# Performance work log

Measured on AMD Instinct MI355X. Metric: run time of the kernel, lower is better.

## Reference

```python
import jax, jax.numpy as jnp
import numpy as np

D_IN = 1024
D_OUT = 1024
NUM_HEADS = 16
HEAD_DIM = D_OUT // NUM_HEADS


def setup_inputs() -> dict:
    key = jax.random.key(0)
    ks = jax.random.split(key, 6)
    b, T = 2, 2048
    scale = 0.02
    x = jax.random.normal(ks[0], (b, T, D_IN), dtype=jnp.float32)
    Wq = jax.random.normal(ks[1], (D_IN, D_OUT), dtype=jnp.float32) * scale
    Wk = jax.random.normal(ks[2], (D_IN, D_OUT), dtype=jnp.float32) * scale
    Wv = jax.random.normal(ks[3], (D_IN, D_OUT), dtype=jnp.float32) * scale
    Wo = jax.random.normal(ks[4], (D_OUT, D_OUT), dtype=jnp.float32) * scale
    bo = jnp.zeros((D_OUT,), dtype=jnp.float32)
    return {"x": x, "Wq": Wq, "Wk": Wk, "Wv": Wv, "Wo": Wo, "bo": bo}


def reference(x, Wq, Wk, Wv, Wo, bo):
    b, T, _ = x.shape
    H, Dh = NUM_HEADS, HEAD_DIM
    # projections: [b,T,d_out] -> [b,H,T,Dh]
    q = (x @ Wq).reshape(b, T, H, Dh).transpose(0, 2, 1, 3)
    k = (x @ Wk).reshape(b, T, H, Dh).transpose(0, 2, 1, 3)
    v = (x @ Wv).reshape(b, T, H, Dh).transpose(0, 2, 1, 3)
    # scores: [b,H,T,T]
    att = jnp.einsum('bhqd,bhkd->bhqk', q, k)
    causal = jnp.triu(jnp.ones((T, T), dtype=bool), k=1)
    att = jnp.where(causal, -jnp.inf, att)
    att = jax.nn.softmax(att / np.sqrt(Dh).astype(np.float32), axis=-1)
    # dropout p=0.0 -> identity
    y = jnp.einsum('bhqk,bhkd->bhqd', att, v)
    y = y.transpose(0, 2, 1, 3).reshape(b, T, H * Dh)
    return y @ Wo + bo
```

## Files before the change

kernel.cpp:

```cpp
#include <hip/hip_runtime.h>

#define T_   2048
#define DM   1024
#define H_   16
#define DH   64

typedef unsigned short u16;
typedef unsigned int u32;
typedef __attribute__((ext_vector_type(8))) short bf16x8;
typedef __attribute__((ext_vector_type(8))) unsigned short u16x8;
typedef __attribute__((ext_vector_type(4))) float f32x4;
typedef __attribute__((ext_vector_type(16))) float f32x16;
typedef __attribute__((ext_vector_type(4))) unsigned int u32x4;
typedef __attribute__((ext_vector_type(2))) unsigned int u32x2;

static __device__ __forceinline__ u16 f2b(float f) {
  unsigned int u = __builtin_bit_cast(unsigned int, f);
  u += 0x7fff + ((u >> 16) & 1);
  return (u16)(u >> 16);
}

static __device__ __forceinline__ u32 cvtpk(float a, float b) {
  u32 d;
  asm("v_cvt_pk_bf16_f32 %0, %1, %2" : "=v"(d) : "v"(a), "v"(b));
  return d;
}

static __device__ __forceinline__ void gll16(const void* g, void* l) {
  __builtin_amdgcn_global_load_lds(
      (const __attribute__((address_space(1))) unsigned int*)g,
      (__attribute__((address_space(3))) unsigned int*)l, 16, 0, 0);
}

static __device__ __forceinline__ bf16x8 ldf(const char* base, int rho,
                                             int k16) {
  return *(const bf16x8*)(base + rho * 128 + ((k16 ^ (rho & 7)) << 4));
}


__global__ __launch_bounds__(256) void k_cvt_x(const float* __restrict__ x,
                                               u16* __restrict__ o) {
  int i = (blockIdx.x * 256 + threadIdx.x) * 8;
  float4 a = *(const float4*)(x + i);
  float4 b = *(const float4*)(x + i + 4);
  u16x8 r;
  r[0] = f2b(a.x); r[1] = f2b(a.y); r[2] = f2b(a.z); r[3] = f2b(a.w);
  r[4] = f2b(b.x); r[5] = f2b(b.y); r[6] = f2b(b.z); r[7] = f2b(b.w);
  *(u16x8*)(o + i) = r;
}

__global__ __launch_bounds__(256) void k_cvt_wt(
    const float* __restrict__ Wq, const float* __restrict__ Wk,
    const float* __restrict__ Wv, const float* __restrict__ Wo,
    u16* __restrict__ oq, u16* __restrict__ ok, u16* __restrict__ ov,
    u16* __restrict__ oo) {
  const float* W; u16* Wt;
  int z = blockIdx.z;
  if (z == 0)      { W = Wq; Wt = oq; }
  else if (z == 1) { W = Wk; Wt = ok; }
  else if (z == 2) { W = Wv; Wt = ov; }
  else             { W = Wo; Wt = oo; }
  const float wsc = (z == 0) ? 0.1803368801111204f : 1.0f;
  __shared__ u16 tile[64][65];
  int k0 = blockIdx.x * 64, n0 = blockIdx.y * 64;
  int r = threadIdx.x >> 2, c0 = (threadIdx.x & 3) * 16;
  const float* src = W + (k0 + r) * DM + n0 + c0;
#pragma unroll
  for (int e = 0; e < 16; e += 4) {
    float4 v = *(const float4*)(src + e);
    tile[r][c0 + e + 0] = f2b(v.x * wsc);
    tile[r][c0 + e + 1] = f2b(v.y * wsc);
    tile[r][c0 + e + 2] = f2b(v.z * wsc);
    tile[r][c0 + e + 3] = f2b(v.w * wsc);
  }
  __syncthreads();
  u16x8 a, b;
#pragma unroll
  for (int e = 0; e < 8; ++e) a[e] = tile[c0 + e][r];
#pragma unroll
  for (int e = 0; e < 8; ++e) b[e] = tile[c0 + 8 + e][r];
  u16* dst = Wt + (n0 + r) * DM + k0 + c0;
  *(u16x8*)dst = a;
  *(u16x8*)(dst + 8) = b;
}

__global__ __launch_bounds__(256) void k_qkv(
    const u16* __restrict__ X, const u16* __restrict__ Wqt,
    const u16* __restrict__ Wkt, const u16* __restrict__ Wvt,
    u16* __restrict__ Qg, u16* __restrict__ Kg, u16* __restrict__ Vtg) {
  __shared__ char smem[34816];
  char* As = smem;
  char* Bs = smem + 16384;
  const int tid = threadIdx.x, lane = tid & 63, w = tid >> 6;
  const int frow = lane & 15, fk = lane >> 4;
  const int wr = (w >> 1) * 64, wc = (w & 1) * 64;
  const int m0 = blockIdx.x * 128;
  const int by = blockIdx.y;
  const int z = by >> 3, n0 = (by & 7) * 128;
  const u16* Wt = (z == 0) ? Wqt : (z == 1) ? Wkt : Wvt;
  const u16* Ap = X + m0 * DM;
  const u16* Bp = Wt + n0 * DM;
  const int ro = lane >> 3;
  const int ce = ((lane & 7) ^ ro) << 3;

  f32x4 acc[4][4];
#pragma unroll
  for (int mi = 0; mi < 4; ++mi)
#pragma unroll
    for (int ni = 0; ni < 4; ++ni) acc[mi][ni] = (f32x4){0.f, 0.f, 0.f, 0.f};

  for (int k0 = 0; k0 < DM; k0 += 64) {
#pragma unroll
    for (int c = 0; c < 4; ++c) {
      const int g8 = (w * 4 + c) * 8;
      gll16(Ap + (g8 + ro) * DM + k0 + ce, As + g8 * 128);
      gll16(Bp + (g8 + ro) * DM + k0 + ce, Bs + g8 * 128);
    }
    asm volatile("s_waitcnt vmcnt(0)" ::: "memory");
    __syncthreads();
    bf16x8 a[4][2], b[4][2];
#pragma unroll
    for (int mi = 0; mi < 4; ++mi)
#pragma unroll
      for (int kk = 0; kk < 2; ++kk)
        a[mi][kk] = ldf(As, wr + mi * 16 + frow, kk * 4 + fk);
#pragma unroll
    for (int ni = 0; ni < 4; ++ni)
#pragma unroll
      for (int kk = 0; kk < 2; ++kk)
        b[ni][kk] = ldf(Bs, wc + ni * 16 + frow, kk * 4 + fk);
#pragma unroll
    for (int mi = 0; mi < 4; ++mi)
#pragma unroll
      for (int ni = 0; ni < 4; ++ni)
#pragma unroll
        for (int kk = 0; kk < 2; ++kk)
          acc[mi][ni] = __builtin_amdgcn_mfma_f32_16x16x32_bf16(
              a[mi][kk], b[ni][kk], acc[mi][ni], 0, 0, 0);
    __syncthreads();
  }

  if (z < 2) {
    u16* out = (z == 0) ? Qg : Kg;
#pragma unroll
    for (int mi = 0; mi < 4; ++mi)
#pragma unroll
      for (int ni = 0; ni < 4; ++ni)
#pragma unroll
        for (int r = 0; r < 4; ++r) {
          int m = m0 + wr + mi * 16 + fk * 4 + r;
          int nl = n0 + wc + ni * 16 + frow;
          int b = m >> 11, t = m & 2047, h = nl >> 6, d = nl & 63;
          out[((b * H_ + h) * T_ + t) * DH + d] = f2b(acc[mi][ni][r]);
        }
  } else {
    u16* Tl = (u16*)smem;
#pragma unroll
    for (int ni = 0; ni < 4; ++ni) {
      const int n = wc + ni * 16 + frow;
#pragma unroll
      for (int mi = 0; mi < 4; ++mi)
#pragma unroll
        for (int r = 0; r < 4; ++r)
          Tl[n * 136 + wr + mi * 16 + fk * 4 + r] = f2b(acc[mi][ni][r]);
    }
    __syncthreads();
    const int n = tid >> 1, c0 = (tid & 1) * 64;
    const int ng = n0 + n, h = ng >> 6, d = ng & 63;
    const int b = m0 >> 11;
    const int tb = (m0 & 2047) + c0;
    u16* dst = Vtg + ((b * H_ + h) * DH + d) * T_ + tb;
#pragma unroll
    for (int e = 0; e < 8; ++e)
      *(u16x8*)(dst + e * 8) = *(const u16x8*)(Tl + n * 136 + c0 + e * 8);
  }
}

__global__ __launch_bounds__(256) void k_out(
    const u16* __restrict__ Y, const u16* __restrict__ Wot,
    const float* __restrict__ bo, float* __restrict__ out) {
  __shared__ char smem[24576];
  char* As = smem;
  char* Bs = smem + 8192;
  const int tid = threadIdx.x, lane = tid & 63, w = tid >> 6;
  const int frow = lane & 15, fk = lane >> 4;
  const int wr = (w >> 1) * 32, wc = (w & 1) * 64;
  const int m0 = blockIdx.x * 64, n0 = blockIdx.y * 128;
  const u16* Ap = Y + m0 * DM;
  const u16* Bp = Wot + n0 * DM;
  const int ro = lane >> 3;
  const int ce = ((lane & 7) ^ ro) << 3;

  f32x4 acc[2][4];
#pragma unroll
  for (int mi = 0; mi < 2; ++mi)
#pragma unroll
    for (int ni = 0; ni < 4; ++ni) acc[mi][ni] = (f32x4){0.f, 0.f, 0.f, 0.f};

  for (int k0 = 0; k0 < DM; k0 += 64) {
#pragma unroll
    for (int c = 0; c < 2; ++c) {
      const int g8 = (w * 2 + c) * 8;
      gll16(Ap + (g8 + ro) * DM + k0 + ce, As + g8 * 128);
    }
#pragma unroll
    for (int c = 0; c < 4; ++c) {
      const int g8 = (w * 4 + c) * 8;
      gll16(Bp + (g8 + ro) * DM + k0 + ce, Bs + g8 * 128);
    }
    asm volatile("s_waitcnt vmcnt(0)" ::: "memory");
    __syncthreads();
    bf16x8 a[2][2], b[4][2];
#pragma unroll
    for (int mi = 0; mi < 2; ++mi)
#pragma unroll
      for (int kk = 0; kk < 2; ++kk)
        a[mi][kk] = ldf(As, wr + mi * 16 + frow, kk * 4 + fk);
#pragma unroll
    for (int ni = 0; ni < 4; ++ni)
#pragma unroll
      for (int kk = 0; kk < 2; ++kk)
        b[ni][kk] = ldf(Bs, wc + ni * 16 + frow, kk * 4 + fk);
#pragma unroll
    for (int mi = 0; mi < 2; ++mi)
#pragma unroll
      for (int ni = 0; ni < 4; ++ni)
#pragma unroll
        for (int kk = 0; kk < 2; ++kk)
          acc[mi][ni] = __builtin_amdgcn_mfma_f32_16x16x32_bf16(
              a[mi][kk], b[ni][kk], acc[mi][ni], 0, 0, 0);
    __syncthreads();
  }
#pragma unroll
  for (int mi = 0; mi < 2; ++mi)
#pragma unroll
    for (int ni = 0; ni < 4; ++ni)
#pragma unroll
      for (int r = 0; r < 4; ++r) {
        int m = m0 + wr + mi * 16 + fk * 4 + r;
        int n = n0 + wc + ni * 16 + frow;
        out[m * DM + n] = acc[mi][ni][r] + bo[n];
      }
}

__global__ __launch_bounds__(256) void k_attn(
    const u16* __restrict__ Qg, const u16* __restrict__ Kg,
    const u16* __restrict__ Vtg, u16* __restrict__ Yg) {
  __shared__ char Kl[64 * 128];
  __shared__ char Vl[64 * 128];
  const int bh = blockIdx.x;
  const int qt = 15 - blockIdx.y;
  const int q0 = qt * 128;
  const int tid = threadIdx.x, w = tid >> 6, lane = tid & 63;
  const int hi = lane >> 5, qq = lane & 31;
  const u16* Qb = Qg + bh * (T_ * DH);
  const u16* Kb = Kg + bh * (T_ * DH);
  const u16* Vb = Vtg + bh * (DH * T_);
  const int qrow = q0 + w * 32 + qq;

  bf16x8 qf[4];
#pragma unroll
  for (int kb = 0; kb < 4; ++kb)
    qf[kb] = *(const bf16x8*)(Qb + qrow * DH + kb * 16 + hi * 8);

  f32x16 o0, o1;
#pragma unroll
  for (int r = 0; r < 16; ++r) { o0[r] = 0.f; o1[r] = 0.f; }
  float m = -1e30f, lp = 0.f;

  const int nt = 2 * qt + 2;
  const int nfull = 2 * qt + (w >> 1);
  const int sr = tid >> 3, sc = tid & 7;
  const int swz0 = (sr * 128 + sc * 16) ^ ((sr & 7) << 4);
  const int swz1 = ((sr + 32) * 128 + sc * 16) ^ ((sr & 7) << 4);

  u32x4 kr0 = *(const u32x4*)(Kb + sr * DH + sc * 8);
  u32x4 kr1 = *(const u32x4*)(Kb + (sr + 32) * DH + sc * 8);
  u32x4 vr0 = *(const u32x4*)(Vb + sr * T_ + sc * 8);
  u32x4 vr1 = *(const u32x4*)(Vb + (sr + 32) * T_ + sc * 8);

  for (int t = 0; t < nt; ++t) {
    __syncthreads();
    *(u32x4*)(Kl + swz0) = kr0;
    *(u32x4*)(Kl + swz1) = kr1;
    *(u32x4*)(Vl + swz0) = vr0;
    *(u32x4*)(Vl + swz1) = vr1;
    __syncthreads();
    if (t + 1 < nt) {
      const int jn = (t + 1) * 64;
      kr0 = *(const u32x4*)(Kb + (jn + sr) * DH + sc * 8);
      kr1 = *(const u32x4*)(Kb + (jn + sr + 32) * DH + sc * 8);
      vr0 = *(const u32x4*)(Vb + sr * T_ + jn + sc * 8);
      vr1 = *(const u32x4*)(Vb + (sr + 32) * T_ + jn + sc * 8);
    }
    if (t > nfull) continue;
    const int j0 = t * 64;

    f32x16 s0, s1;
#pragma unroll
    for (int r = 0; r < 16; ++r) { s0[r] = 0.f; s1[r] = 0.f; }
#pragma unroll
    for (int kb = 0; kb < 4; ++kb) {
      const int cb = (kb * 2 + hi) * 16;
      bf16x8 ka0 = *(const bf16x8*)(Kl + ((qq * 128 + cb) ^ ((qq & 7) << 4)));
      s0 = __builtin_amdgcn_mfma_f32_32x32x16_bf16(ka0, qf[kb], s0, 0, 0, 0);
      bf16x8 ka1 =
          *(const bf16x8*)(Kl + (((qq + 32) * 128 + cb) ^ ((qq & 7) << 4)));
      s1 = __builtin_amdgcn_mfma_f32_32x32x16_bf16(ka1, qf[kb], s1, 0, 0, 0);
    }
    if (t == nfull) {
#pragma unroll
      for (int r = 0; r < 16; ++r) {
        const int cr = (r & 3) + 8 * (r >> 2) + 4 * hi;
        if (j0 + cr > qrow) s0[r] = -1e30f;
        if (j0 + 32 + cr > qrow) s1[r] = -1e30f;
      }
    }
    float mt = s0[0];
#pragma unroll
    for (int r = 1; r < 16; ++r) mt = fmaxf(mt, s0[r]);
#pragma unroll
    for (int r = 0; r < 16; ++r) mt = fmaxf(mt, s1[r]);
    mt = fmaxf(mt, __shfl_xor(mt, 32));
    if (__any(mt > m + 8.f)) {
      const float mn = fmaxf(m, mt);
      const float al = __builtin_amdgcn_exp2f(m - mn);
      m = mn;
#pragma unroll
      for (int r = 0; r < 16; ++r) { o0[r] *= al; o1[r] *= al; }
      lp *= al;
    }
#pragma unroll
    for (int r = 0; r < 16; ++r) {
      s0[r] = __builtin_amdgcn_exp2f(s0[r] - m);
      s1[r] = __builtin_amdgcn_exp2f(s1[r] - m);
    }
    float ps = 0.f;
#pragma unroll
    for (int r = 0; r < 16; ++r) ps += s0[r] + s1[r];
    lp += ps;
    bf16x8 pb[4];
#define MKCH(DST, S, RB)                                                     \
  {                                                                          \
    u32 a01 = cvtpk(S[RB + 0], S[RB + 1]);                                   \
    u32 a23 = cvtpk(S[RB + 2], S[RB + 3]);                                   \
    u32 a45 = cvtpk(S[RB + 4], S[RB + 5]);                                   \
    u32 a67 = cvtpk(S[RB + 6], S[RB + 7]);                                   \
    asm volatile("v_permlane32_swap_b32 %0, %1" : "+v"(a01), "+v"(a45));     \
    asm volatile("v_permlane32_swap_b32 %0, %1" : "+v"(a23), "+v"(a67));     \
    u32x4 t4;                                                                \
    t4[0] = a01; t4[1] = a23; t4[2] = a45; t4[3] = a67;                      \
    DST = __builtin_bit_cast(bf16x8, t4);                                    \
  }
    MKCH(pb[0], s0, 0)
    MKCH(pb[1], s0, 8)
    MKCH(pb[2], s1, 0)
    MKCH(pb[3], s1, 8)
#undef MKCH
#pragma unroll
    for (int jc = 0; jc < 4; ++jc) {
      const int cb = (jc * 2 + hi) * 16;
      bf16x8 va0 = *(const bf16x8*)(Vl + ((qq * 128 + cb) ^ ((qq & 7) << 4)));
      o0 = __builtin_amdgcn_mfma_f32_32x32x16_bf16(va0, pb[jc], o0, 0, 0, 0);
      bf16x8 va1 =
          *(const bf16x8*)(Vl + (((qq + 32) * 128 + cb) ^ ((qq & 7) << 4)));
      o1 = __builtin_amdgcn_mfma_f32_32x32x16_bf16(va1, pb[jc], o1, 0, 0, 0);
    }
  }
  lp += __shfl_xor(lp, 32);
  const float rl = 1.0f / lp;
  const int obase = ((bh >> 4) * T_ + qrow) * DM + (bh & 15) * DH;
#pragma unroll
  for (int g = 0; g < 4; ++g) {
    u32x2 st;
    st[0] = cvtpk(o0[g * 4 + 0] * rl, o0[g * 4 + 1] * rl);
    st[1] = cvtpk(o0[g * 4 + 2] * rl, o0[g * 4 + 3] * rl);
    *(u32x2*)(Yg + obase + g * 8 + hi * 4) = st;
    st[0] = cvtpk(o1[g * 4 + 0] * rl, o1[g * 4 + 1] * rl);
    st[1] = cvtpk(o1[g * 4 + 2] * rl, o1[g * 4 + 3] * rl);
    *(u32x2*)(Yg + obase + 32 + g * 8 + hi * 4) = st;
  }
}


extern "C" void kernel_launch(void* const* d_in, const int* in_sizes, int n_in,
                              void* d_out, int out_size, void* d_ws,
                              size_t ws_size, hipStream_t stream) {
  const float* x  = (const float*)d_in[0];
  const float* Wq = (const float*)d_in[1];
  const float* Wk = (const float*)d_in[2];
  const float* Wv = (const float*)d_in[3];
  const float* Wo = (const float*)d_in[4];
  const float* bo = (const float*)d_in[5];
  float* out = (float*)d_out;
  char* ws = (char*)d_ws;

  u16* xb  = (u16*)(ws);
  u16* wqt = (u16*)(ws + (8ull << 20));
  u16* wkt = (u16*)(ws + (10ull << 20));
  u16* wvt = (u16*)(ws + (12ull << 20));
  u16* wot = (u16*)(ws + (14ull << 20));
  u16* Qg  = (u16*)(ws + (16ull << 20));
  u16* Kg  = (u16*)(ws + (24ull << 20));
  u16* Vtg = (u16*)(ws + (32ull << 20));
  u16* Yg  = (u16*)(ws + (40ull << 20));

  k_cvt_x<<<2048, 256, 0, stream>>>(x, xb);
  k_cvt_wt<<<dim3(16, 16, 4), 256, 0, stream>>>(Wq, Wk, Wv, Wo, wqt, wkt, wvt, wot);
  k_qkv<<<dim3(32, 24), 256, 0, stream>>>(xb, wqt, wkt, wvt, Qg, Kg, Vtg);
  k_attn<<<dim3(32, 16), 256, 0, stream>>>(Qg, Kg, Vtg, Yg);
  k_out<<<dim3(64, 8), 256, 0, stream>>>(Yg, wot, bo, out);
}
```

Measured before the change: 118.3 us.

## Double-buffer K/V in LDS with 128-key tiles and single barrier per step

The attention kernel's key tile grows from 64 to 128 keys, and the K and V tiles in LDS are double-buffered. Each step now needs one barrier instead of two, and the next tile is written to the alternate buffer after the PV MFMAs. The per-wave skip of fully masked tiles is dropped, so every wave masks on the last (diagonal) tile. This halves the loop trip count and barrier overhead but quadruples LDS use to 64KB per block, raises register pressure (four score accumulators, eight P fragments), and adds some wasted masked compute on the diagonal.

```diff
diff --git a/kernel.cpp b/kernel.cpp
--- a/kernel.cpp
+++ b/kernel.cpp
@@ -246,8 +246,8 @@
 __global__ __launch_bounds__(256) void k_attn(
     const u16* __restrict__ Qg, const u16* __restrict__ Kg,
     const u16* __restrict__ Vtg, u16* __restrict__ Yg) {
-  __shared__ char Kl[64 * 128];
-  __shared__ char Vl[64 * 128];
+  __shared__ char Kl[2][16384];
+  __shared__ char Vl[2][16384];
   const int bh = blockIdx.x;
   const int qt = 15 - blockIdx.y;
   const int q0 = qt * 128;
@@ -268,59 +268,68 @@
   for (int r = 0; r < 16; ++r) { o0[r] = 0.f; o1[r] = 0.f; }
   float m = -1e30f, lp = 0.f;
 
-  const int nt = 2 * qt + 2;
-  const int nfull = 2 * qt + (w >> 1);
-  const int sr = tid >> 3, sc = tid & 7;
-  const int swz0 = (sr * 128 + sc * 16) ^ ((sr & 7) << 4);
-  const int swz1 = ((sr + 32) * 128 + sc * 16) ^ ((sr & 7) << 4);
-
-  u32x4 kr0 = *(const u32x4*)(Kb + sr * DH + sc * 8);
-  u32x4 kr1 = *(const u32x4*)(Kb + (sr + 32) * DH + sc * 8);
-  u32x4 vr0 = *(const u32x4*)(Vb + sr * T_ + sc * 8);
-  u32x4 vr1 = *(const u32x4*)(Vb + (sr + 32) * T_ + sc * 8);
+  const int nt = qt + 1;
+  const int ksr = tid >> 1, kc4 = (tid & 1) * 4;
+  const int vdr = tid >> 2, vc4 = (tid & 3) * 4;
+  int kwo[4], vwo[4];
+#pragma unroll
+  for (int c = 0; c < 4; ++c) {
+    kwo[c] = ksr * 128 + (((kc4 + c) ^ (ksr & 7)) << 4);
+    vwo[c] = vdr * 256 + (((vc4 + c) ^ (vdr & 15)) << 4);
+  }
+
+  u32x4 kr[4], vr[4];
+#pragma unroll
+  for (int c = 0; c < 4; ++c)
+    kr[c] = *(const u32x4*)(Kb + ksr * DH + (kc4 + c) * 8);
+#pragma unroll
+  for (int c = 0; c < 4; ++c)
+    vr[c] = *(const u32x4*)(Vb + vdr * T_ + (vc4 + c) * 8);
+#pragma unroll
+  for (int c = 0; c < 4; ++c) *(u32x4*)(Kl[0] + kwo[c]) = kr[c];
+#pragma unroll
+  for (int c = 0; c < 4; ++c) *(u32x4*)(Vl[0] + vwo[c]) = vr[c];
+  __syncthreads();
 
   for (int t = 0; t < nt; ++t) {
-    __syncthreads();
-    *(u32x4*)(Kl + swz0) = kr0;
-    *(u32x4*)(Kl + swz1) = kr1;
-    *(u32x4*)(Vl + swz0) = vr0;
-    *(u32x4*)(Vl + swz1) = vr1;
-    __syncthreads();
+    const char* Kc = Kl[t & 1];
+    const char* Vc = Vl[t & 1];
     if (t + 1 < nt) {
-      const int jn = (t + 1) * 64;
-      kr0 = *(const u32x4*)(Kb + (jn + sr) * DH + sc * 8);
-      kr1 = *(const u32x4*)(Kb + (jn + sr + 32) * DH + sc * 8);
-      vr0 = *(const u32x4*)(Vb + sr * T_ + jn + sc * 8);
-      vr1 = *(const u32x4*)(Vb + (sr + 32) * T_ + jn + sc * 8);
-    }
-    if (t > nfull) continue;
-    const int j0 = t * 64;
-
-    f32x16 s0, s1;
-#pragma unroll
-    for (int r = 0; r < 16; ++r) { s0[r] = 0.f; s1[r] = 0.f; }
-#pragma unroll
-    for (int kb = 0; kb < 4; ++kb) {
-      const int cb = (kb * 2 + hi) * 16;
-      bf16x8 ka0 = *(const bf16x8*)(Kl + ((qq * 128 + cb) ^ ((qq & 7) << 4)));
-      s0 = __builtin_amdgcn_mfma_f32_32x32x16_bf16(ka0, qf[kb], s0, 0, 0, 0);
-      bf16x8 ka1 =
-          *(const bf16x8*)(Kl + (((qq + 32) * 128 + cb) ^ ((qq & 7) << 4)));
-      s1 = __builtin_amdgcn_mfma_f32_32x32x16_bf16(ka1, qf[kb], s1, 0, 0, 0);
-    }
-    if (t == nfull) {
-#pragma unroll
-      for (int r = 0; r < 16; ++r) {
-        const int cr = (r & 3) + 8 * (r >> 2) + 4 * hi;
-        if (j0 + cr > qrow) s0[r] = -1e30f;
-        if (j0 + 32 + cr > qrow) s1[r] = -1e30f;
+      const int jn = (t + 1) * 128;
+#pragma unroll
+      for (int c = 0; c < 4; ++c)
+        kr[c] = *(const u32x4*)(Kb + (jn + ksr) * DH + (kc4 + c) * 8);
+#pragma unroll
+      for (int c = 0; c < 4; ++c)
+        vr[c] = *(const u32x4*)(Vb + vdr * T_ + jn + (vc4 + c) * 8);
+    }
+
+    f32x16 s[4];
+#pragma unroll
+    for (int jg = 0; jg < 4; ++jg) {
+#pragma unroll
+      for (int r = 0; r < 16; ++r) s[jg][r] = 0.f;
+#pragma unroll
+      for (int kb = 0; kb < 4; ++kb) {
+        bf16x8 ka = *(const bf16x8*)(
+            Kc + (jg * 32 + qq) * 128 + (((kb * 2 + hi) ^ (qq & 7)) << 4));
+        s[jg] = __builtin_amdgcn_mfma_f32_32x32x16_bf16(ka, qf[kb], s[jg], 0, 0, 0);
       }
     }
-    float mt = s0[0];
-#pragma unroll
-    for (int r = 1; r < 16; ++r) mt = fmaxf(mt, s0[r]);
-#pragma unroll
-    for (int r = 0; r < 16; ++r) mt = fmaxf(mt, s1[r]);
+    if (t == nt - 1) {
+#pragma unroll
+      for (int jg = 0; jg < 4; ++jg)
+#pragma unroll
+        for (int r = 0; r < 16; ++r) {
+          const int j = q0 + jg * 32 + (r & 3) + 8 * (r >> 2) + 4 * hi;
+          if (j > qrow) s[jg][r] = -1e30f;
+        }
+    }
+    float mt = s[0][0];
+#pragma unroll
+    for (int jg = 0; jg < 4; ++jg)
+#pragma unroll
+      for (int r = 0; r < 16; ++r) mt = fmaxf(mt, s[jg][r]);
     mt = fmaxf(mt, __shfl_xor(mt, 32));
     if (__any(mt > m + 8.f)) {
       const float mn = fmaxf(m, mt);
@@ -330,16 +339,16 @@
       for (int r = 0; r < 16; ++r) { o0[r] *= al; o1[r] *= al; }
       lp *= al;
     }
-#pragma unroll
-    for (int r = 0; r < 16; ++r) {
-      s0[r] = __builtin_amdgcn_exp2f(s0[r] - m);
-      s1[r] = __builtin_amdgcn_exp2f(s1[r] - m);
-    }
     float ps = 0.f;
 #pragma unroll
-    for (int r = 0; r < 16; ++r) ps += s0[r] + s1[r];
+    for (int jg = 0; jg < 4; ++jg)
+#pragma unroll
+      for (int r = 0; r < 16; ++r) {
+        s[jg][r] = __builtin_amdgcn_exp2f(s[jg][r] - m);
+        ps += s[jg][r];
+      }
     lp += ps;
-    bf16x8 pb[4];
+    bf16x8 pb[8];
 #define MKCH(DST, S, RB)                                                     \
   {                                                                          \
     u32 a01 = cvtpk(S[RB + 0], S[RB + 1]);                                   \
@@ -352,20 +361,29 @@
     t4[0] = a01; t4[1] = a23; t4[2] = a45; t4[3] = a67;                      \
     DST = __builtin_bit_cast(bf16x8, t4);                                    \
   }
-    MKCH(pb[0], s0, 0)
-    MKCH(pb[1], s0, 8)
-    MKCH(pb[2], s1, 0)
-    MKCH(pb[3], s1, 8)
+    MKCH(pb[0], s[0], 0) MKCH(pb[1], s[0], 8)
+    MKCH(pb[2], s[1], 0) MKCH(pb[3], s[1], 8)
+    MKCH(pb[4], s[2], 0) MKCH(pb[5], s[2], 8)
+    MKCH(pb[6], s[3], 0) MKCH(pb[7], s[3], 8)
 #undef MKCH
 #pragma unroll
-    for (int jc = 0; jc < 4; ++jc) {
-      const int cb = (jc * 2 + hi) * 16;
-      bf16x8 va0 = *(const bf16x8*)(Vl + ((qq * 128 + cb) ^ ((qq & 7) << 4)));
+    for (int jc = 0; jc < 8; ++jc) {
+      bf16x8 va0 = *(const bf16x8*)(
+          Vc + qq * 256 + (((jc * 2 + hi) ^ (qq & 15)) << 4));
       o0 = __builtin_amdgcn_mfma_f32_32x32x16_bf16(va0, pb[jc], o0, 0, 0, 0);
-      bf16x8 va1 =
-          *(const bf16x8*)(Vl + (((qq + 32) * 128 + cb) ^ ((qq & 7) << 4)));
+      bf16x8 va1 = *(const bf16x8*)(
+          Vc + (qq + 32) * 256 + (((jc * 2 + hi) ^ (qq & 15)) << 4));
       o1 = __builtin_amdgcn_mfma_f32_32x32x16_bf16(va1, pb[jc], o1, 0, 0, 0);
     }
+    if (t + 1 < nt) {
+      char* Kn = Kl[(t + 1) & 1];
+      char* Vn = Vl[(t + 1) & 1];
+#pragma unroll
+      for (int c = 0; c < 4; ++c) *(u32x4*)(Kn + kwo[c]) = kr[c];
+#pragma unroll
+      for (int c = 0; c < 4; ++c) *(u32x4*)(Vn + vwo[c]) = vr[c];
+    }
+    __syncthreads();
   }
   lp += __shfl_xor(lp, 32);
   const float rl = 1.0f / lp;
```

Measured after the change: 124.1 us. 1.05x slower.

## Double-buffer attention K/V tiles via direct global-to-LDS loads with smaller blocks

Applied to the files above, without the earlier changes.

The attention kernel now uses 128-thread blocks covering 64 query rows, giving twice as many blocks and removing the idle-wave masked tiles of the old 128-row layout. K/V tiles are loaded straight from global memory into a double-buffered LDS with swizzled addresses (gll16), so the next tile loads while the current one is computed, and each iteration needs one barrier instead of two. The row max and row sum reductions become tree reductions to shorten dependency chains. The cost is twice the LDS per block and more blocks re-reading Q/K/V, and correctness depends on the gll16 helper and the new swizzle matching the read pattern.

```diff
diff --git a/kernel.cpp b/kernel.cpp
--- a/kernel.cpp
+++ b/kernel.cpp
@@ -243,14 +243,14 @@
       }
 }
 
-__global__ __launch_bounds__(256) void k_attn(
+__global__ __launch_bounds__(128) void k_attn(
     const u16* __restrict__ Qg, const u16* __restrict__ Kg,
     const u16* __restrict__ Vtg, u16* __restrict__ Yg) {
-  __shared__ char Kl[64 * 128];
-  __shared__ char Vl[64 * 128];
+  __shared__ char Kl[2][8192];
+  __shared__ char Vl[2][8192];
   const int bh = blockIdx.x;
-  const int qt = 15 - blockIdx.y;
-  const int q0 = qt * 128;
+  const int qt = 31 - blockIdx.y;
+  const int q0 = qt * 64;
   const int tid = threadIdx.x, w = tid >> 6, lane = tid & 63;
   const int hi = lane >> 5, qq = lane & 31;
   const u16* Qb = Qg + bh * (T_ * DH);
@@ -268,60 +268,62 @@
   for (int r = 0; r < 16; ++r) { o0[r] = 0.f; o1[r] = 0.f; }
   float m = -1e30f, lp = 0.f;
 
-  const int nt = 2 * qt + 2;
-  const int nfull = 2 * qt + (w >> 1);
-  const int sr = tid >> 3, sc = tid & 7;
-  const int swz0 = (sr * 128 + sc * 16) ^ ((sr & 7) << 4);
-  const int swz1 = ((sr + 32) * 128 + sc * 16) ^ ((sr & 7) << 4);
-
-  u32x4 kr0 = *(const u32x4*)(Kb + sr * DH + sc * 8);
-  u32x4 kr1 = *(const u32x4*)(Kb + (sr + 32) * DH + sc * 8);
-  u32x4 vr0 = *(const u32x4*)(Vb + sr * T_ + sc * 8);
-  u32x4 vr1 = *(const u32x4*)(Vb + (sr + 32) * T_ + sc * 8);
+  const int nt = qt + 1;
+  const int ro = lane >> 3;
+  const int ce = ((lane & 7) ^ ro) << 3;
+
+#pragma unroll
+  for (int c = 0; c < 4; ++c) {
+    const int g = w * 4 + c;
+    gll16(Kb + (g * 8 + ro) * DH + ce, Kl[0] + g * 1024);
+    gll16(Vb + (g * 8 + ro) * T_ + ce, Vl[0] + g * 1024);
+  }
+  asm volatile("s_waitcnt vmcnt(0)" ::: "memory");
+  __syncthreads();
 
   for (int t = 0; t < nt; ++t) {
-    __syncthreads();
-    *(u32x4*)(Kl + swz0) = kr0;
-    *(u32x4*)(Kl + swz1) = kr1;
-    *(u32x4*)(Vl + swz0) = vr0;
-    *(u32x4*)(Vl + swz1) = vr1;
-    __syncthreads();
+    const char* Kc = Kl[t & 1];
+    const char* Vc = Vl[t & 1];
     if (t + 1 < nt) {
       const int jn = (t + 1) * 64;
-      kr0 = *(const u32x4*)(Kb + (jn + sr) * DH + sc * 8);
-      kr1 = *(const u32x4*)(Kb + (jn + sr + 32) * DH + sc * 8);
-      vr0 = *(const u32x4*)(Vb + sr * T_ + jn + sc * 8);
-      vr1 = *(const u32x4*)(Vb + (sr + 32) * T_ + jn + sc * 8);
-    }
-    if (t > nfull) continue;
-    const int j0 = t * 64;
+      char* Kn = Kl[(t + 1) & 1];
+      char* Vn = Vl[(t + 1) & 1];
+#pragma unroll
+      for (int c = 0; c < 4; ++c) {
+        const int g = w * 4 + c;
+        gll16(Kb + (jn + g * 8 + ro) * DH + ce, Kn + g * 1024);
+        gll16(Vb + (g * 8 + ro) * T_ + jn + ce, Vn + g * 1024);
+      }
+    }
 
     f32x16 s0, s1;
 #pragma unroll
     for (int r = 0; r < 16; ++r) { s0[r] = 0.f; s1[r] = 0.f; }
 #pragma unroll
     for (int kb = 0; kb < 4; ++kb) {
-      const int cb = (kb * 2 + hi) * 16;
-      bf16x8 ka0 = *(const bf16x8*)(Kl + ((qq * 128 + cb) ^ ((qq & 7) << 4)));
+      bf16x8 ka0 = *(const bf16x8*)(
+          Kc + qq * 128 + (((kb * 2 + hi) ^ (qq & 7)) << 4));
       s0 = __builtin_amdgcn_mfma_f32_32x32x16_bf16(ka0, qf[kb], s0, 0, 0, 0);
-      bf16x8 ka1 =
-          *(const bf16x8*)(Kl + (((qq + 32) * 128 + cb) ^ ((qq & 7) << 4)));
+      bf16x8 ka1 = *(const bf16x8*)(
+          Kc + (qq + 32) * 128 + (((kb * 2 + hi) ^ (qq & 7)) << 4));
       s1 = __builtin_amdgcn_mfma_f32_32x32x16_bf16(ka1, qf[kb], s1, 0, 0, 0);
     }
-    if (t == nfull) {
+    if (t == nt - 1) {
 #pragma unroll
       for (int r = 0; r < 16; ++r) {
-        const int cr = (r & 3) + 8 * (r >> 2) + 4 * hi;
-        if (j0 + cr > qrow) s0[r] = -1e30f;
-        if (j0 + 32 + cr > qrow) s1[r] = -1e30f;
+        const int cr = q0 + (r & 3) + 8 * (r >> 2) + 4 * hi;
+        if (cr > qrow) s0[r] = -1e30f;
+        if (cr + 32 > qrow) s1[r] = -1e30f;
       }
     }
-    float mt = s0[0];
-#pragma unroll
-    for (int r = 1; r < 16; ++r) mt = fmaxf(mt, s0[r]);
-#pragma unroll
-    for (int r = 0; r < 16; ++r) mt = fmaxf(mt, s1[r]);
-    mt = fmaxf(mt, __shfl_xor(mt, 32));
+    float tm[16];
+#pragma unroll
+    for (int r = 0; r < 16; ++r) tm[r] = fmaxf(s0[r], s1[r]);
+#pragma unroll
+    for (int st = 8; st > 0; st >>= 1)
+#pragma unroll
+      for (int r = 0; r < st; ++r) tm[r] = fmaxf(tm[r], tm[r + st]);
+    const float mt = fmaxf(tm[0], __shfl_xor(tm[0], 32));
     if (__any(mt > m + 8.f)) {
       const float mn = fmaxf(m, mt);
       const float al = __builtin_amdgcn_exp2f(m - mn);
@@ -330,15 +332,18 @@
       for (int r = 0; r < 16; ++r) { o0[r] *= al; o1[r] *= al; }
       lp *= al;
     }
+    float ts[16];
 #pragma unroll
     for (int r = 0; r < 16; ++r) {
       s0[r] = __builtin_amdgcn_exp2f(s0[r] - m);
       s1[r] = __builtin_amdgcn_exp2f(s1[r] - m);
-    }
-    float ps = 0.f;
-#pragma unroll
-    for (int r = 0; r < 16; ++r) ps += s0[r] + s1[r];
-    lp += ps;
+      ts[r] = s0[r] + s1[r];
+    }
+#pragma unroll
+    for (int st = 8; st > 0; st >>= 1)
+#pragma unroll
+      for (int r = 0; r < st; ++r) ts[r] += ts[r + st];
+    lp += ts[0];
     bf16x8 pb[4];
 #define MKCH(DST, S, RB)                                                     \
   {                                                                          \
@@ -359,13 +364,15 @@
 #undef MKCH
 #pragma unroll
     for (int jc = 0; jc < 4; ++jc) {
-      const int cb = (jc * 2 + hi) * 16;
-      bf16x8 va0 = *(const bf16x8*)(Vl + ((qq * 128 + cb) ^ ((qq & 7) << 4)));
+      bf16x8 va0 = *(const bf16x8*)(
+          Vc + qq * 128 + (((jc * 2 + hi) ^ (qq & 7)) << 4));
       o0 = __builtin_amdgcn_mfma_f32_32x32x16_bf16(va0, pb[jc], o0, 0, 0, 0);
-      bf16x8 va1 =
-          *(const bf16x8*)(Vl + (((qq + 32) * 128 + cb) ^ ((qq & 7) << 4)));
+      bf16x8 va1 = *(const bf16x8*)(
+          Vc + (qq + 32) * 128 + (((jc * 2 + hi) ^ (qq & 7)) << 4));
       o1 = __builtin_amdgcn_mfma_f32_32x32x16_bf16(va1, pb[jc], o1, 0, 0, 0);
     }
+    asm volatile("s_waitcnt vmcnt(0)" ::: "memory");
+    __syncthreads();
   }
   lp += __shfl_xor(lp, 32);
   const float rl = 1.0f / lp;
@@ -408,6 +415,6 @@
   k_cvt_x<<<2048, 256, 0, stream>>>(x, xb);
   k_cvt_wt<<<dim3(16, 16, 4), 256, 0, stream>>>(Wq, Wk, Wv, Wo, wqt, wkt, wvt, wot);
   k_qkv<<<dim3(32, 24), 256, 0, stream>>>(xb, wqt, wkt, wvt, Qg, Kg, Vtg);
-  k_attn<<<dim3(32, 16), 256, 0, stream>>>(Qg, Kg, Vtg, Yg);
+  k_attn<<<dim3(32, 32), 128, 0, stream>>>(Qg, Kg, Vtg, Yg);
   k_out<<<dim3(64, 8), 256, 0, stream>>>(Yg, wot, bo, out);
 }
```

New measurement: 124.5 us. +5.3%, slower.

## Restructure attention into single-wave blocks loading K/V directly to registers

Applied to the files above, without the earlier changes.

The attention kernel now runs 64-thread blocks, each handling 32 query rows, instead of 256-thread blocks sharing K/V tiles through LDS. K and V fragments are loaded straight from global memory into registers, with the next K tile double-buffered, which removes the LDS staging and the block-wide barriers. The max and sum reductions become tree reductions. The cost is that each wave re-reads K/V from global/L2 with no sharing across waves, and it uses more registers for the fragment buffers.

```diff
diff --git a/kernel.cpp b/kernel.cpp
--- a/kernel.cpp
+++ b/kernel.cpp
@@ -11,7 +11,6 @@
 typedef __attribute__((ext_vector_type(8))) unsigned short u16x8;
 typedef __attribute__((ext_vector_type(4))) float f32x4;
 typedef __attribute__((ext_vector_type(16))) float f32x16;
-typedef __attribute__((ext_vector_type(4))) unsigned int u32x4;
 typedef __attribute__((ext_vector_type(2))) unsigned int u32x2;
 
 static __device__ __forceinline__ u16 f2b(float f) {
@@ -243,20 +242,18 @@
       }
 }
 
-__global__ __launch_bounds__(256) void k_attn(
+__global__ __launch_bounds__(64) void k_attn(
     const u16* __restrict__ Qg, const u16* __restrict__ Kg,
     const u16* __restrict__ Vtg, u16* __restrict__ Yg) {
-  __shared__ char Kl[64 * 128];
-  __shared__ char Vl[64 * 128];
   const int bh = blockIdx.x;
-  const int qt = 15 - blockIdx.y;
-  const int q0 = qt * 128;
-  const int tid = threadIdx.x, w = tid >> 6, lane = tid & 63;
+  const int qt = 63 - blockIdx.y;
+  const int q0 = qt * 32;
+  const int lane = threadIdx.x;
   const int hi = lane >> 5, qq = lane & 31;
   const u16* Qb = Qg + bh * (T_ * DH);
   const u16* Kb = Kg + bh * (T_ * DH);
   const u16* Vb = Vtg + bh * (DH * T_);
-  const int qrow = q0 + w * 32 + qq;
+  const int qrow = q0 + qq;
 
   bf16x8 qf[4];
 #pragma unroll
@@ -268,78 +265,68 @@
   for (int r = 0; r < 16; ++r) { o0[r] = 0.f; o1[r] = 0.f; }
   float m = -1e30f, lp = 0.f;
 
-  const int nt = 2 * qt + 2;
-  const int nfull = 2 * qt + (w >> 1);
-  const int sr = tid >> 3, sc = tid & 7;
-  const int swz0 = (sr * 128 + sc * 16) ^ ((sr & 7) << 4);
-  const int swz1 = ((sr + 32) * 128 + sc * 16) ^ ((sr & 7) << 4);
-
-  u32x4 kr0 = *(const u32x4*)(Kb + sr * DH + sc * 8);
-  u32x4 kr1 = *(const u32x4*)(Kb + (sr + 32) * DH + sc * 8);
-  u32x4 vr0 = *(const u32x4*)(Vb + sr * T_ + sc * 8);
-  u32x4 vr1 = *(const u32x4*)(Vb + (sr + 32) * T_ + sc * 8);
-
-  for (int t = 0; t < nt; ++t) {
-    __syncthreads();
-    *(u32x4*)(Kl + swz0) = kr0;
-    *(u32x4*)(Kl + swz1) = kr1;
-    *(u32x4*)(Vl + swz0) = vr0;
-    *(u32x4*)(Vl + swz1) = vr1;
-    __syncthreads();
-    if (t + 1 < nt) {
-      const int jn = (t + 1) * 64;
-      kr0 = *(const u32x4*)(Kb + (jn + sr) * DH + sc * 8);
-      kr1 = *(const u32x4*)(Kb + (jn + sr + 32) * DH + sc * 8);
-      vr0 = *(const u32x4*)(Vb + sr * T_ + jn + sc * 8);
-      vr1 = *(const u32x4*)(Vb + (sr + 32) * T_ + jn + sc * 8);
-    }
-    if (t > nfull) continue;
-    const int j0 = t * 64;
-
-    f32x16 s0, s1;
-#pragma unroll
-    for (int r = 0; r < 16; ++r) { s0[r] = 0.f; s1[r] = 0.f; }
-#pragma unroll
-    for (int kb = 0; kb < 4; ++kb) {
-      const int cb = (kb * 2 + hi) * 16;
-      bf16x8 ka0 = *(const bf16x8*)(Kl + ((qq * 128 + cb) ^ ((qq & 7) << 4)));
-      s0 = __builtin_amdgcn_mfma_f32_32x32x16_bf16(ka0, qf[kb], s0, 0, 0, 0);
-      bf16x8 ka1 =
-          *(const bf16x8*)(Kl + (((qq + 32) * 128 + cb) ^ ((qq & 7) << 4)));
-      s1 = __builtin_amdgcn_mfma_f32_32x32x16_bf16(ka1, qf[kb], s1, 0, 0, 0);
-    }
-    if (t == nfull) {
-#pragma unroll
-      for (int r = 0; r < 16; ++r) {
-        const int cr = (r & 3) + 8 * (r >> 2) + 4 * hi;
-        if (j0 + cr > qrow) s0[r] = -1e30f;
-        if (j0 + 32 + cr > qrow) s1[r] = -1e30f;
-      }
-    }
-    float mt = s0[0];
-#pragma unroll
-    for (int r = 1; r < 16; ++r) mt = fmaxf(mt, s0[r]);
-#pragma unroll
-    for (int r = 0; r < 16; ++r) mt = fmaxf(mt, s1[r]);
-    mt = fmaxf(mt, __shfl_xor(mt, 32));
-    if (__any(mt > m + 8.f)) {
-      const float mn = fmaxf(m, mt);
-      const float al = __builtin_amdgcn_exp2f(m - mn);
-      m = mn;
-#pragma unroll
-      for (int r = 0; r < 16; ++r) { o0[r] *= al; o1[r] *= al; }
-      lp *= al;
-    }
-#pragma unroll
-    for (int r = 0; r < 16; ++r) {
-      s0[r] = __builtin_amdgcn_exp2f(s0[r] - m);
-      s1[r] = __builtin_amdgcn_exp2f(s1[r] - m);
-    }
-    float ps = 0.f;
-#pragma unroll
-    for (int r = 0; r < 16; ++r) ps += s0[r] + s1[r];
-    lp += ps;
-    bf16x8 pb[4];
+  const int nt = (qt >> 1) + 1;
+
+#define LOADK(KF, J0)                                                        \
+  _Pragma("unroll") for (int i = 0; i < 4; ++i) {                            \
+    KF[i] = *(const bf16x8*)(Kb + ((J0) + qq) * DH + (i * 2 + hi) * 8);      \
+    KF[4 + i] = *(const bf16x8*)(Kb + ((J0) + qq + 32) * DH + (i * 2 + hi) * 8); \
+  }
+#define LOADV(VF, J0)                                                        \
+  _Pragma("unroll") for (int i = 0; i < 4; ++i) {                            \
+    VF[i] = *(const bf16x8*)(Vb + qq * T_ + (J0) + (i * 2 + hi) * 8);        \
+    VF[4 + i] = *(const bf16x8*)(Vb + (qq + 32) * T_ + (J0) + (i * 2 + hi) * 8); \
+  }
+
+#define PROCESS(KF, VF, T)                                                   \
+  {                                                                          \
+    f32x16 s0, s1;                                                           \
+    _Pragma("unroll") for (int r = 0; r < 16; ++r) { s0[r] = 0.f; s1[r] = 0.f; } \
+    _Pragma("unroll") for (int kb = 0; kb < 4; ++kb) {                       \
+      s0 = __builtin_amdgcn_mfma_f32_32x32x16_bf16(KF[kb], qf[kb], s0, 0, 0, 0); \
+      s1 = __builtin_amdgcn_mfma_f32_32x32x16_bf16(KF[4 + kb], qf[kb], s1, 0, 0, 0); \
+    }                                                                        \
+    if ((T) == nt - 1) {                                                     \
+      const int j0m = (T) * 64;                                              \
+      _Pragma("unroll") for (int r = 0; r < 16; ++r) {                       \
+        const int cr = j0m + (r & 3) + 8 * (r >> 2) + 4 * hi;                \
+        if (cr > qrow) s0[r] = -1e30f;                                       \
+        if (cr + 32 > qrow) s1[r] = -1e30f;                                  \
+      }                                                                      \
+    }                                                                        \
+    float tm[16];                                                            \
+    _Pragma("unroll") for (int r = 0; r < 16; ++r) tm[r] = fmaxf(s0[r], s1[r]); \
+    _Pragma("unroll") for (int stp = 8; stp > 0; stp >>= 1)                  \
+        _Pragma("unroll") for (int r = 0; r < stp; ++r)                      \
+            tm[r] = fmaxf(tm[r], tm[r + stp]);                               \
+    const float mt = fmaxf(tm[0], __shfl_xor(tm[0], 32));                    \
+    if (__any(mt > m + 8.f)) {                                               \
+      const float mn = fmaxf(m, mt);                                         \
+      const float al = __builtin_amdgcn_exp2f(m - mn);                       \
+      m = mn;                                                                \
+      _Pragma("unroll") for (int r = 0; r < 16; ++r) { o0[r] *= al; o1[r] *= al; } \
+      lp *= al;                                                              \
+    }                                                                        \
+    float ts[16];                                                            \
+    _Pragma("unroll") for (int r = 0; r < 16; ++r) {                         \
+      s0[r] = __builtin_amdgcn_exp2f(s0[r] - m);                             \
+      s1[r] = __builtin_amdgcn_exp2f(s1[r] - m);                             \
+      ts[r] = s0[r] + s1[r];                                                 \
+    }                                                                        \
+    _Pragma("unroll") for (int stp = 8; stp > 0; stp >>= 1)                  \
+        _Pragma("unroll") for (int r = 0; r < stp; ++r) ts[r] += ts[r + stp]; \
+    lp += ts[0];                                                             \
+    bf16x8 pb[4];                                                            \
+    MKCH(pb[0], s0, 0)                                                       \
+    MKCH(pb[1], s0, 8)                                                       \
+    MKCH(pb[2], s1, 0)                                                       \
+    MKCH(pb[3], s1, 8)                                                       \
+    _Pragma("unroll") for (int jc = 0; jc < 4; ++jc) {                       \
+      o0 = __builtin_amdgcn_mfma_f32_32x32x16_bf16(VF[jc], pb[jc], o0, 0, 0, 0); \
+      o1 = __builtin_amdgcn_mfma_f32_32x32x16_bf16(VF[4 + jc], pb[jc], o1, 0, 0, 0); \
+    }                                                                        \
+  }
+
 #define MKCH(DST, S, RB)                                                     \
   {                                                                          \
     u32 a01 = cvtpk(S[RB + 0], S[RB + 1]);                                   \
@@ -348,25 +335,29 @@
     u32 a67 = cvtpk(S[RB + 6], S[RB + 7]);                                   \
     asm volatile("v_permlane32_swap_b32 %0, %1" : "+v"(a01), "+v"(a45));     \
     asm volatile("v_permlane32_swap_b32 %0, %1" : "+v"(a23), "+v"(a67));     \
-    u32x4 t4;                                                                \
+    u32x4_t t4;                                                              \
     t4[0] = a01; t4[1] = a23; t4[2] = a45; t4[3] = a67;                      \
     DST = __builtin_bit_cast(bf16x8, t4);                                    \
   }
-    MKCH(pb[0], s0, 0)
-    MKCH(pb[1], s0, 8)
-    MKCH(pb[2], s1, 0)
-    MKCH(pb[3], s1, 8)
+  typedef __attribute__((ext_vector_type(4))) unsigned int u32x4_t;
+
+  bf16x8 kA[8], kB[8], vv[8];
+  LOADK(kA, 0)
+  for (int t = 0; t < nt; t += 2) {
+    if (t + 1 < nt) LOADK(kB, (t + 1) * 64)
+    LOADV(vv, t * 64)
+    PROCESS(kA, vv, t)
+    if (t + 1 < nt) {
+      if (t + 2 < nt) LOADK(kA, (t + 2) * 64)
+      LOADV(vv, (t + 1) * 64)
+      PROCESS(kB, vv, t + 1)
+    }
+  }
+#undef PROCESS
 #undef MKCH
-#pragma unroll
-    for (int jc = 0; jc < 4; ++jc) {
-      const int cb = (jc * 2 + hi) * 16;
-      bf16x8 va0 = *(const bf16x8*)(Vl + ((qq * 128 + cb) ^ ((qq & 7) << 4)));
-      o0 = __builtin_amdgcn_mfma_f32_32x32x16_bf16(va0, pb[jc], o0, 0, 0, 0);
-      bf16x8 va1 =
-          *(const bf16x8*)(Vl + (((qq + 32) * 128 + cb) ^ ((qq & 7) << 4)));
-      o1 = __builtin_amdgcn_mfma_f32_32x32x16_bf16(va1, pb[jc], o1, 0, 0, 0);
-    }
-  }
+#undef LOADK
+#undef LOADV
+
   lp += __shfl_xor(lp, 32);
   const float rl = 1.0f / lp;
   const int obase = ((bh >> 4) * T_ + qrow) * DM + (bh & 15) * DH;
@@ -408,6 +399,6 @@
   k_cvt_x<<<2048, 256, 0, stream>>>(x, xb);
   k_cvt_wt<<<dim3(16, 16, 4), 256, 0, stream>>>(Wq, Wk, Wv, Wo, wqt, wkt, wvt, wot);
   k_qkv<<<dim3(32, 24), 256, 0, stream>>>(xb, wqt, wkt, wvt, Qg, Kg, Vtg);
-  k_attn<<<dim3(32, 16), 256, 0, stream>>>(Qg, Kg, Vtg, Yg);
+  k_attn<<<dim3(32, 64), 64, 0, stream>>>(Qg, Kg, Vtg, Yg);
   k_out<<<dim3(64, 8), 256, 0, stream>>>(Yg, wot, bo, out);
 }
```

Result: slower. 145.5 us (+23.0%).
